# Optimization experiments

Measured on AMD Instinct MI355X. Metric: run time of the kernel, lower is better.

Reference implementation:

```python
import jax, jax.numpy as jnp
import numpy as np

B = 262144
HIST = 24
FORE = 20
HID = 256
# torch: tau_int = clamp(tau,1,18).long().item(); default tau=6.0 -> static 6 (host sync in torch)
TAU_INT = 6


def setup_inputs() -> dict:
    key = jax.random.key(0)
    ks = jax.random.split(key, 9)
    s = 0.1
    return {
        "history": jax.random.normal(ks[0], (B, HIST), jnp.float32),
        "enc_w1": jax.random.normal(ks[1], (HIST + FORE, HID), jnp.float32) * s,
        "enc_b1": jnp.zeros((HID,), jnp.float32),
        "enc_w2": jax.random.normal(ks[2], (HID, HID), jnp.float32) * s,
        "enc_b2": jnp.zeros((HID,), jnp.float32),
        "cor_w1": jax.random.normal(ks[3], (HID, HID), jnp.float32) * s,
        "cor_b1": jnp.zeros((HID,), jnp.float32),
        "cor_w2": jax.random.normal(ks[4], (HID, FORE), jnp.float32) * s,
        "cor_b2": jnp.zeros((FORE,), jnp.float32),
        "alpha": jnp.float32(0.2),
        "beta": jnp.float32(0.3),
        "gamma": jnp.float32(0.01),
        "tau": jnp.float32(6.0),
        "lambda_mix": jnp.float32(0.5),
    }


def _physics_core(history, alpha, beta, gamma, steps):
    a = jax.nn.sigmoid(alpha)
    b = jax.nn.sigmoid(beta)
    g = jnp.abs(gamma)
    T0 = history[:, -1]                      # [B]
    buf0 = history[:, -TAU_INT:].T           # [tau, B]; buf0[0] = history[:, -tau]

    def step(carry, _):
        T, buf = carry
        T_delayed = buf[0]
        T_new = T - a * T - b * T_delayed - g * T ** 3
        buf = jnp.concatenate([buf[1:], T_new[None, :]], axis=0)
        return (T_new, buf), T_new

    _, preds = jax.lax.scan(step, (T0, buf0), None, length=steps)
    return preds.T                            # [B, steps]


def reference(history, enc_w1, enc_b1, enc_w2, enc_b2,
              cor_w1, cor_b1, cor_w2, cor_b2,
              alpha, beta, gamma, tau, lambda_mix):
    T_physics = _physics_core(history, alpha, beta, gamma, FORE)   # [B, FORE]
    combined = jnp.concatenate([history, T_physics], axis=1)       # [B, HIST+FORE]
    h = jnp.tanh(combined @ enc_w1 + enc_b1)
    features = jnp.tanh(h @ enc_w2 + enc_b2)
    c = jnp.tanh(features @ cor_w1 + cor_b1)
    T_soft = c @ cor_w2 + cor_b2                                   # [B, FORE]
    lam = jax.nn.sigmoid(lambda_mix)
    T_pred = T_physics + lam * T_soft
    return (T_pred, T_physics, T_soft)
```

## Files before the change

kernel.cpp:

```cpp
#include <hip/hip_runtime.h>
#include <hip/hip_bf16.h>

#define NROWS 262144
#define HISTC 24
#define FOREC 20
#define BROWS 128

typedef __bf16        v8bf __attribute__((ext_vector_type(8)));
typedef float         v4f  __attribute__((ext_vector_type(4)));
typedef float         v2f  __attribute__((ext_vector_type(2)));
typedef unsigned int  v4u  __attribute__((ext_vector_type(4)));
typedef unsigned int  v2u  __attribute__((ext_vector_type(2)));

#define WS_WT1_OFF 64
#define WT1_ELEMS 16384
#define WT2_ELEMS 65536
#define WT3_ELEMS 65536
#define WT4R_ELEMS 65536

#define TANH_C 2.885390081777927f

__device__ __forceinline__ unsigned short f2bf(float x) {
    unsigned u = __builtin_bit_cast(unsigned, x);
    u += 0x7FFFu + ((u >> 16) & 1u);
    return (unsigned short)(u >> 16);
}

__device__ __forceinline__ unsigned packbf2(float a, float b) {
    unsigned ua = __builtin_bit_cast(unsigned, a) + 0x8000u;
    unsigned ub = __builtin_bit_cast(unsigned, b) + 0x8000u;
    return __builtin_amdgcn_perm(ub, ua, 0x07060302u);
}

__device__ __forceinline__ void lds_barrier() {
    asm volatile("s_waitcnt lgkmcnt(0)\n\ts_barrier" ::: "memory");
}

__device__ __forceinline__ int swzi(int r, int byteoff) {
    return (r << 8) + (((byteoff) ^ ((r & 7) << 4)) >> 1);
}

__global__ void prep_kernel(const float* __restrict__ w1, const float* __restrict__ w2,
                            const float* __restrict__ w3, const float* __restrict__ w4,
                            const float* __restrict__ alpha, const float* __restrict__ beta,
                            const float* __restrict__ gamma, const float* __restrict__ lmix,
                            unsigned char* __restrict__ ws)
{
    if (blockIdx.x == 104) {
        int t = threadIdx.x;
        float* wsf = (float*)ws;
        if (t == 0) wsf[0] = 1.0f / (1.0f + expf(-alpha[0]));
        else if (t == 1) wsf[1] = 1.0f / (1.0f + expf(-beta[0]));
        else if (t == 2) wsf[2] = fabsf(gamma[0]);
        else if (t == 3) wsf[3] = 1.0f / (1.0f + expf(-lmix[0]));
        return;
    }
    int idx = (blockIdx.x * 256 + threadIdx.x) * 8;
    const float* src;
    int KT, Kreal, Nreal, srcN, local, ntmask;
    unsigned short* dst = (unsigned short*)(ws + WS_WT1_OFF);
    if (idx < WT1_ELEMS) {
        local = idx; src = w1; KT = 2; Kreal = 44; Nreal = 256; srcN = 256; ntmask = 255;
    } else if (idx < WT1_ELEMS + WT2_ELEMS) {
        local = idx - WT1_ELEMS; dst += WT1_ELEMS;
        src = w2; KT = 8; Kreal = 256; Nreal = 256; srcN = 256; ntmask = 255;
    } else if (idx < WT1_ELEMS + WT2_ELEMS + WT3_ELEMS) {
        local = idx - (WT1_ELEMS + WT2_ELEMS); dst += WT1_ELEMS + WT2_ELEMS;
        src = w3; KT = 8; Kreal = 256; Nreal = 256; srcN = 256; ntmask = 255;
    } else {
        local = idx - (WT1_ELEMS + WT2_ELEMS + WT3_ELEMS);
        dst += WT1_ELEMS + WT2_ELEMS + WT3_ELEMS;
        src = w4; KT = 8; Kreal = 256; Nreal = 20; srcN = 20; ntmask = 1;
    }
    int L   = (local >> 3) & 63;
    int blk = local >> 9;
    int kt = blk % KT, nt = (blk / KT) & ntmask;
    int cc = L & 15,  qq = L >> 4;
    int feat = nt * 16 + cc;
    int kbase = kt * 32 + qq * 8;
    unsigned short tmp[8];
#pragma unroll
    for (int j = 0; j < 8; ++j) {
        int k = kbase + j;
        float v = (k < Kreal && feat < Nreal) ? src[k * srcN + feat] : 0.0f;
        tmp[j] = f2bf(v);
    }
    v4u pk;
    pk[0] = tmp[0] | ((unsigned)tmp[1] << 16);
    pk[1] = tmp[2] | ((unsigned)tmp[3] << 16);
    pk[2] = tmp[4] | ((unsigned)tmp[5] << 16);
    pk[3] = tmp[6] | ((unsigned)tmp[7] << 16);
    *(v4u*)&dst[local] = pk;
}

template<int KT, int KTN>
__device__ __forceinline__ void layer_pipe(char* bufc,
        const v4u* __restrict__ wp, const v4u* __restrict__ wpn,
        const float* __restrict__ bias, v4u A[2][4],
        int be0, int bo0, const int* wfx,
        int w, int q, int lane)
{
    v4f acc[4][8];
#pragma unroll
    for (int ft = 0; ft < 4; ++ft)
#pragma unroll
        for (int st = 0; st < 8; ++st) {
            v4f z = {0.0f, 0.0f, 0.0f, 0.0f};
            acc[ft][st] = z;
        }

    v4u Bf[2][4];
#pragma unroll
    for (int j = 0; j < 4; ++j)
        Bf[0][j] = *(const v4u*)(bufc + be0 + j * 8192);

#pragma unroll
    for (int kt = 0; kt < KT; ++kt) {
        const int cs = kt & 1;
        const int ps = cs ^ 1;
        if (kt + 1 < KT) {
#pragma unroll
            for (int ft = 0; ft < 4; ++ft)
                A[ps][ft] = wp[((w * 4 + ft) * KT + kt + 1) * 64 + lane];
        } else {
#pragma unroll
            for (int ft = 0; ft < 4; ++ft)
                A[ps][ft] = wpn[((w * 4 + ft) * KTN + 0) * 64 + lane];
        }
        {
            const int rb = cs ? bo0 : be0;
#pragma unroll
            for (int j = 0; j < 4; ++j)
                Bf[1][j] = *(const v4u*)(bufc + rb + (4 + j) * 8192 + kt * 64);
        }
        __builtin_amdgcn_s_setprio(1);
#pragma unroll
        for (int j = 0; j < 4; ++j) {
            v8bf bb = __builtin_bit_cast(v8bf, Bf[0][j]);
#pragma unroll
            for (int ft = 0; ft < 4; ++ft)
                acc[ft][j] = __builtin_amdgcn_mfma_f32_16x16x32_bf16(
                    __builtin_bit_cast(v8bf, A[cs][ft]), bb, acc[ft][j], 0, 0, 0);
        }
        __builtin_amdgcn_s_setprio(0);
        if (kt + 1 < KT) {
            const int rb = ps ? bo0 : be0;
#pragma unroll
            for (int j = 0; j < 4; ++j)
                Bf[0][j] = *(const v4u*)(bufc + rb + j * 8192 + (kt + 1) * 64);
        }
        __builtin_amdgcn_s_setprio(1);
#pragma unroll
        for (int j = 0; j < 4; ++j) {
            v8bf bb = __builtin_bit_cast(v8bf, Bf[1][j]);
#pragma unroll
            for (int ft = 0; ft < 4; ++ft)
                acc[ft][4 + j] = __builtin_amdgcn_mfma_f32_16x16x32_bf16(
                    __builtin_bit_cast(v8bf, A[cs][ft]), bb, acc[ft][4 + j], 0, 0, 0);
        }
        __builtin_amdgcn_s_setprio(0);
    }

    lds_barrier();

    const v2f C2   = {TANH_C, TANH_C};
    const v2f one2 = {1.0f, 1.0f};
    const v2f m22  = {-2.0f, -2.0f};
#pragma unroll
    for (int ft = 0; ft < 4; ++ft) {
        v4f bi = *(const v4f*)&bias[w * 64 + ft * 16 + q * 4];
        v2f bi01 = {bi[0], bi[1]}, bi23 = {bi[2], bi[3]};
        v2f bic01 = bi01 * C2, bic23 = bi23 * C2;
#pragma unroll
        for (int st = 0; st < 8; ++st) {
            v4f a = acc[ft][st];
            v2f a01 = {a[0], a[1]}, a23 = {a[2], a[3]};
            v2f t01 = __builtin_elementwise_fma(a01, C2, bic01);
            v2f t23 = __builtin_elementwise_fma(a23, C2, bic23);
            v2f p01, p23;
            p01[0] = __builtin_amdgcn_exp2f(t01[0]);
            p01[1] = __builtin_amdgcn_exp2f(t01[1]);
            p23[0] = __builtin_amdgcn_exp2f(t23[0]);
            p23[1] = __builtin_amdgcn_exp2f(t23[1]);
            v2f d01 = p01 + one2;
            v2f d23 = p23 + one2;
            v2f rc01, rc23;
            rc01[0] = __builtin_amdgcn_rcpf(d01[0]);
            rc01[1] = __builtin_amdgcn_rcpf(d01[1]);
            rc23[0] = __builtin_amdgcn_rcpf(d23[0]);
            rc23[1] = __builtin_amdgcn_rcpf(d23[1]);
            v2f x01 = __builtin_elementwise_fma(rc01, m22, one2);
            v2f x23 = __builtin_elementwise_fma(rc23, m22, one2);
            v2u d; d[0] = packbf2(x01[0], x01[1]); d[1] = packbf2(x23[0], x23[1]);
            *(v2u*)(bufc + wfx[ft] + st * 8192) = d;
        }
    }
    lds_barrier();
}

__global__ __launch_bounds__(256, 2) void fused_kernel(
    const float* __restrict__ history,
    const float* __restrict__ eb1, const float* __restrict__ eb2,
    const float* __restrict__ cb1, const float* __restrict__ cb2,
    const unsigned char* __restrict__ ws, float* __restrict__ out)
{
    __shared__ unsigned short buf[BROWS * 256];
    __shared__ float tp[BROWS * 20];
    char* bufc = (char*)buf;

    const int tid  = threadIdx.x;
    const int w    = tid >> 6;
    const int lane = tid & 63;
    const int c    = lane & 15;
    const int q    = lane >> 4;
    const int row0 = blockIdx.x << 7;
    const float* wsf = (const float*)ws;
    const v4u* wp1 = (const v4u*)(ws + WS_WT1_OFF);
    const v4u* wp2 = wp1 + WT1_ELEMS / 8;
    const v4u* wp3 = wp2 + WT2_ELEMS / 8;
    const v4u* wp4 = wp3 + WT3_ELEMS / 8;

    const int e    = (c >> 2) & 1;
    const int d64  = e << 6;
    const int qp_r = (q * 16) ^ ((c & 3) << 4);
    const int be0  = c * 512 + qp_r + d64;
    const int bo0  = c * 512 + qp_r - d64;
    int wfx[4];
#pragma unroll
    for (int ft = 0; ft < 4; ++ft)
        wfx[ft] = c * 512 + w * 128 + ((ft * 32 + q * 8) ^ ((c & 7) << 4));

    v4u A[2][4];
#pragma unroll
    for (int ft = 0; ft < 4; ++ft)
        A[0][ft] = wp1[((w * 4 + ft) * 2 + 0) * 64 + lane];

#pragma unroll
    for (int i = 0; i < 3; ++i) {
        int e2 = tid + i * 256;
        int r  = e2 / 6, c4 = e2 - r * 6;
        v4f h4 = *(const v4f*)&history[(long)(row0 + r) * 24 + c4 * 4];
        v2u d; d[0] = packbf2(h4[0], h4[1]); d[1] = packbf2(h4[2], h4[3]);
        *(v2u*)&buf[swzi(r, c4 * 8)] = d;
    }
#pragma unroll
    for (int i = 0; i < 3; ++i) {
        int e2 = tid + i * 256;
        if (e2 < 640) {
            int r = e2 / 5, g = e2 - r * 5;
            v2u z = {0u, 0u};
            *(v2u*)&buf[swzi(r, 88 + g * 8)] = z;
        }
    }
    if (tid < BROWS) {
        const float* hrow = &history[(long)(row0 + tid) * 24];
        v2f h18 = *(const v2f*)&hrow[18];
        v4f h20 = *(const v4f*)&hrow[20];
        float pa = wsf[0], pb = wsf[1], pg = wsf[2];
        float d0 = h18[0], d1 = h18[1], d2 = h20[0];
        float d3 = h20[1], d4 = h20[2], d5 = h20[3];
        float T = d5;
#pragma unroll
        for (int s = 0; s < 20; ++s) {
            float t3 = T * T * T;
            float Tn = T - pa * T;
            Tn = Tn - pb * d0;
            Tn = Tn - pg * t3;
            tp[tid * 20 + s] = Tn;
            buf[swzi(tid, 48 + 2 * s)] = f2bf(Tn);
            d0 = d1; d1 = d2; d2 = d3; d3 = d4; d4 = d5; d5 = Tn;
            T = Tn;
        }
    }
    lds_barrier();

    layer_pipe<2, 8>(bufc, wp1, wp2, eb1, A, be0, bo0, wfx, w, q, lane);
    layer_pipe<8, 8>(bufc, wp2, wp3, eb2, A, be0, bo0, wfx, w, q, lane);
    layer_pipe<8, 8>(bufc, wp3, wp4, cb1, A, be0, bo0, wfx, w, q, lane);

    const int b4e = be0 + w * 16384;
    const int b4o = bo0 + w * 16384;
    v4f a4[2][2];
#pragma unroll
    for (int s2 = 0; s2 < 2; ++s2)
#pragma unroll
        for (int ft = 0; ft < 2; ++ft) {
            v4f z = {0.0f, 0.0f, 0.0f, 0.0f};
            a4[s2][ft] = z;
        }
    v4u Aw[2][2];
    Aw[0][0] = A[0][0]; Aw[0][1] = A[0][1];
    v4u B4[2][2];
    B4[0][0] = *(const v4u*)(bufc + b4e);
    B4[0][1] = *(const v4u*)(bufc + b4e + 8192);
#pragma unroll
    for (int kt = 0; kt < 8; ++kt) {
        const int cs = kt & 1, ps = cs ^ 1;
        if (kt + 1 < 8) {
            Aw[ps][0] = wp4[((w * 4 + 0) * 8 + kt + 1) * 64 + lane];
            Aw[ps][1] = wp4[((w * 4 + 1) * 8 + kt + 1) * 64 + lane];
            const int rb = ps ? b4o : b4e;
            B4[ps][0] = *(const v4u*)(bufc + rb + (kt + 1) * 64);
            B4[ps][1] = *(const v4u*)(bufc + rb + 8192 + (kt + 1) * 64);
        }
#pragma unroll
        for (int s2 = 0; s2 < 2; ++s2) {
            v8bf bb = __builtin_bit_cast(v8bf, B4[cs][s2]);
#pragma unroll
            for (int ft = 0; ft < 2; ++ft)
                a4[s2][ft] = __builtin_amdgcn_mfma_f32_16x16x32_bf16(
                    __builtin_bit_cast(v8bf, Aw[cs][ft]), bb, a4[s2][ft], 0, 0, 0);
        }
    }

    const float lam = wsf[3];
    float* outP = out;
    float* outF = out + (long)NROWS * 20;
    float* outS = out + (long)NROWS * 40;
#pragma unroll
    for (int s2 = 0; s2 < 2; ++s2) {
        const int trow = (w * 2 + s2) * 16 + c;
        const long sample = (long)row0 + trow;
        {
            int f0 = q * 4;
            v4f bi  = *(const v4f*)&cb2[f0];
            v4f tph = *(const v4f*)&tp[trow * 20 + f0];
            v4f ts, pr;
#pragma unroll
            for (int r = 0; r < 4; ++r) {
                ts[r] = a4[s2][0][r] + bi[r];
                pr[r] = tph[r] + lam * ts[r];
            }
            *(v4f*)&outS[sample * 20 + f0] = ts;
            *(v4f*)&outP[sample * 20 + f0] = pr;
            *(v4f*)&outF[sample * 20 + f0] = tph;
        }
        if (q == 0) {
            v4f bi  = *(const v4f*)&cb2[16];
            v4f tph = *(const v4f*)&tp[trow * 20 + 16];
            v4f ts, pr;
#pragma unroll
            for (int r = 0; r < 4; ++r) {
                ts[r] = a4[s2][1][r] + bi[r];
                pr[r] = tph[r] + lam * ts[r];
            }
            *(v4f*)&outS[sample * 20 + 16] = ts;
            *(v4f*)&outP[sample * 20 + 16] = pr;
            *(v4f*)&outF[sample * 20 + 16] = tph;
        }
    }
}

extern "C" void kernel_launch(void* const* d_in, const int* in_sizes, int n_in,
                              void* d_out, int out_size, void* d_ws, size_t ws_size,
                              hipStream_t stream)
{
    const float* history = (const float*)d_in[0];
    const float* enc_w1  = (const float*)d_in[1];
    const float* enc_b1  = (const float*)d_in[2];
    const float* enc_w2  = (const float*)d_in[3];
    const float* enc_b2  = (const float*)d_in[4];
    const float* cor_w1  = (const float*)d_in[5];
    const float* cor_b1  = (const float*)d_in[6];
    const float* cor_w2  = (const float*)d_in[7];
    const float* cor_b2  = (const float*)d_in[8];
    const float* alpha   = (const float*)d_in[9];
    const float* beta    = (const float*)d_in[10];
    const float* gamma   = (const float*)d_in[11];
    const float* lmix    = (const float*)d_in[13];

    prep_kernel<<<105, 256, 0, stream>>>(enc_w1, enc_w2, cor_w1, cor_w2,
                                         alpha, beta, gamma, lmix,
                                         (unsigned char*)d_ws);
    fused_kernel<<<NROWS / BROWS, 256, 0, stream>>>(history, enc_b1, enc_b2,
                                                    cor_b1, cor_b2,
                                                    (const unsigned char*)d_ws,
                                                    (float*)d_out);
}
```

Before: 201.0 us.

## Double rows per block to 256 with 512 threads, halving per-wave feature tiles

```diff
diff --git a/kernel.cpp b/kernel.cpp
--- a/kernel.cpp
+++ b/kernel.cpp
@@ -4,7 +4,7 @@
 #define NROWS 262144
 #define HISTC 24
 #define FOREC 20
-#define BROWS 128
+#define BROWS 256
 
 typedef __bf16        v8bf __attribute__((ext_vector_type(8)));
 typedef float         v4f  __attribute__((ext_vector_type(4)));
@@ -96,15 +96,15 @@
 template<int KT, int KTN>
 __device__ __forceinline__ void layer_pipe(char* bufc,
         const v4u* __restrict__ wp, const v4u* __restrict__ wpn,
-        const float* __restrict__ bias, v4u A[2][4],
+        const float* __restrict__ bias, v4u A[2][2],
         int be0, int bo0, const int* wfx,
         int w, int q, int lane)
 {
-    v4f acc[4][8];
-#pragma unroll
-    for (int ft = 0; ft < 4; ++ft)
-#pragma unroll
-        for (int st = 0; st < 8; ++st) {
+    v4f acc[2][16];
+#pragma unroll
+    for (int ft = 0; ft < 2; ++ft)
+#pragma unroll
+        for (int st = 0; st < 16; ++st) {
             v4f z = {0.0f, 0.0f, 0.0f, 0.0f};
             acc[ft][st] = z;
         }
@@ -116,49 +116,42 @@
 
 #pragma unroll
     for (int kt = 0; kt < KT; ++kt) {
+        const int rb = (kt & 1) ? bo0 : be0;
         const int cs = kt & 1;
         const int ps = cs ^ 1;
         if (kt + 1 < KT) {
 #pragma unroll
-            for (int ft = 0; ft < 4; ++ft)
-                A[ps][ft] = wp[((w * 4 + ft) * KT + kt + 1) * 64 + lane];
+            for (int ft = 0; ft < 2; ++ft)
+                A[ps][ft] = wp[((w * 2 + ft) * KT + kt + 1) * 64 + lane];
         } else {
 #pragma unroll
-            for (int ft = 0; ft < 4; ++ft)
-                A[ps][ft] = wpn[((w * 4 + ft) * KTN + 0) * 64 + lane];
-        }
-        {
-            const int rb = cs ? bo0 : be0;
-#pragma unroll
-            for (int j = 0; j < 4; ++j)
-                Bf[1][j] = *(const v4u*)(bufc + rb + (4 + j) * 8192 + kt * 64);
-        }
-        __builtin_amdgcn_s_setprio(1);
-#pragma unroll
-        for (int j = 0; j < 4; ++j) {
-            v8bf bb = __builtin_bit_cast(v8bf, Bf[0][j]);
-#pragma unroll
-            for (int ft = 0; ft < 4; ++ft)
-                acc[ft][j] = __builtin_amdgcn_mfma_f32_16x16x32_bf16(
-                    __builtin_bit_cast(v8bf, A[cs][ft]), bb, acc[ft][j], 0, 0, 0);
-        }
-        __builtin_amdgcn_s_setprio(0);
-        if (kt + 1 < KT) {
-            const int rb = ps ? bo0 : be0;
-#pragma unroll
-            for (int j = 0; j < 4; ++j)
-                Bf[0][j] = *(const v4u*)(bufc + rb + j * 8192 + (kt + 1) * 64);
-        }
-        __builtin_amdgcn_s_setprio(1);
-#pragma unroll
-        for (int j = 0; j < 4; ++j) {
-            v8bf bb = __builtin_bit_cast(v8bf, Bf[1][j]);
-#pragma unroll
-            for (int ft = 0; ft < 4; ++ft)
-                acc[ft][4 + j] = __builtin_amdgcn_mfma_f32_16x16x32_bf16(
-                    __builtin_bit_cast(v8bf, A[cs][ft]), bb, acc[ft][4 + j], 0, 0, 0);
-        }
-        __builtin_amdgcn_s_setprio(0);
+            for (int ft = 0; ft < 2; ++ft)
+                A[ps][ft] = wpn[((w * 2 + ft) * KTN + 0) * 64 + lane];
+        }
+#pragma unroll
+        for (int g = 0; g < 4; ++g) {
+            const int cur = g & 1;
+            if (g + 1 < 4) {
+#pragma unroll
+                for (int j = 0; j < 4; ++j)
+                    Bf[cur ^ 1][j] = *(const v4u*)(bufc + rb + ((g + 1) * 4 + j) * 8192 + kt * 64);
+            } else if (kt + 1 < KT) {
+                const int rbn = ((kt + 1) & 1) ? bo0 : be0;
+#pragma unroll
+                for (int j = 0; j < 4; ++j)
+                    Bf[cur ^ 1][j] = *(const v4u*)(bufc + rbn + j * 8192 + (kt + 1) * 64);
+            }
+            __builtin_amdgcn_s_setprio(1);
+#pragma unroll
+            for (int j = 0; j < 4; ++j) {
+                v8bf bb = __builtin_bit_cast(v8bf, Bf[cur][j]);
+#pragma unroll
+                for (int ft = 0; ft < 2; ++ft)
+                    acc[ft][g * 4 + j] = __builtin_amdgcn_mfma_f32_16x16x32_bf16(
+                        __builtin_bit_cast(v8bf, A[cs][ft]), bb, acc[ft][g * 4 + j], 0, 0, 0);
+            }
+            __builtin_amdgcn_s_setprio(0);
+        }
     }
 
     lds_barrier();
@@ -167,12 +160,12 @@
     const v2f one2 = {1.0f, 1.0f};
     const v2f m22  = {-2.0f, -2.0f};
 #pragma unroll
-    for (int ft = 0; ft < 4; ++ft) {
-        v4f bi = *(const v4f*)&bias[w * 64 + ft * 16 + q * 4];
+    for (int ft = 0; ft < 2; ++ft) {
+        v4f bi = *(const v4f*)&bias[w * 32 + ft * 16 + q * 4];
         v2f bi01 = {bi[0], bi[1]}, bi23 = {bi[2], bi[3]};
         v2f bic01 = bi01 * C2, bic23 = bi23 * C2;
 #pragma unroll
-        for (int st = 0; st < 8; ++st) {
+        for (int st = 0; st < 16; ++st) {
             v4f a = acc[ft][st];
             v2f a01 = {a[0], a[1]}, a23 = {a[2], a[3]};
             v2f t01 = __builtin_elementwise_fma(a01, C2, bic01);
@@ -198,7 +191,7 @@
     lds_barrier();
 }
 
-__global__ __launch_bounds__(256, 2) void fused_kernel(
+__global__ __launch_bounds__(512, 2) void fused_kernel(
     const float* __restrict__ history,
     const float* __restrict__ eb1, const float* __restrict__ eb2,
     const float* __restrict__ cb1, const float* __restrict__ cb2,
@@ -213,7 +206,7 @@
     const int lane = tid & 63;
     const int c    = lane & 15;
     const int q    = lane >> 4;
-    const int row0 = blockIdx.x << 7;
+    const int row0 = blockIdx.x << 8;
     const float* wsf = (const float*)ws;
     const v4u* wp1 = (const v4u*)(ws + WS_WT1_OFF);
     const v4u* wp2 = wp1 + WT1_ELEMS / 8;
@@ -225,19 +218,19 @@
     const int qp_r = (q * 16) ^ ((c & 3) << 4);
     const int be0  = c * 512 + qp_r + d64;
     const int bo0  = c * 512 + qp_r - d64;
-    int wfx[4];
-#pragma unroll
-    for (int ft = 0; ft < 4; ++ft)
-        wfx[ft] = c * 512 + w * 128 + ((ft * 32 + q * 8) ^ ((c & 7) << 4));
-
-    v4u A[2][4];
-#pragma unroll
-    for (int ft = 0; ft < 4; ++ft)
-        A[0][ft] = wp1[((w * 4 + ft) * 2 + 0) * 64 + lane];
+    int wfx[2];
+#pragma unroll
+    for (int ft = 0; ft < 2; ++ft)
+        wfx[ft] = c * 512 + ((w * 64 + ft * 32 + q * 8) ^ ((c & 7) << 4));
+
+    v4u A[2][2];
+#pragma unroll
+    for (int ft = 0; ft < 2; ++ft)
+        A[0][ft] = wp1[((w * 2 + ft) * 2 + 0) * 64 + lane];
 
 #pragma unroll
     for (int i = 0; i < 3; ++i) {
-        int e2 = tid + i * 256;
+        int e2 = tid + i * 512;
         int r  = e2 / 6, c4 = e2 - r * 6;
         v4f h4 = *(const v4f*)&history[(long)(row0 + r) * 24 + c4 * 4];
         v2u d; d[0] = packbf2(h4[0], h4[1]); d[1] = packbf2(h4[2], h4[3]);
@@ -245,8 +238,8 @@
     }
 #pragma unroll
     for (int i = 0; i < 3; ++i) {
-        int e2 = tid + i * 256;
-        if (e2 < 640) {
+        int e2 = tid + i * 512;
+        if (e2 < 1280) {
             int r = e2 / 5, g = e2 - r * 5;
             v2u z = {0u, 0u};
             *(v2u*)&buf[swzi(r, 88 + g * 8)] = z;
@@ -297,8 +290,8 @@
     for (int kt = 0; kt < 8; ++kt) {
         const int cs = kt & 1, ps = cs ^ 1;
         if (kt + 1 < 8) {
-            Aw[ps][0] = wp4[((w * 4 + 0) * 8 + kt + 1) * 64 + lane];
-            Aw[ps][1] = wp4[((w * 4 + 1) * 8 + kt + 1) * 64 + lane];
+            Aw[ps][0] = wp4[((w * 2 + 0) * 8 + kt + 1) * 64 + lane];
+            Aw[ps][1] = wp4[((w * 2 + 1) * 8 + kt + 1) * 64 + lane];
             const int rb = ps ? b4o : b4e;
             B4[ps][0] = *(const v4u*)(bufc + rb + (kt + 1) * 64);
             B4[ps][1] = *(const v4u*)(bufc + rb + 8192 + (kt + 1) * 64);
@@ -372,7 +365,7 @@
     prep_kernel<<<105, 256, 0, stream>>>(enc_w1, enc_w2, cor_w1, cor_w2,
                                          alpha, beta, gamma, lmix,
                                          (unsigned char*)d_ws);
-    fused_kernel<<<NROWS / BROWS, 256, 0, stream>>>(history, enc_b1, enc_b2,
+    fused_kernel<<<NROWS / BROWS, 512, 0, stream>>>(history, enc_b1, enc_b2,
                                                     cor_b1, cor_b2,
                                                     (const unsigned char*)d_ws,
                                                     (float*)d_out);
```

Result: slower. 207.7 us (+3.3%).
